# Kernel tuning notes

Hardware: AMD Instinct MI355X
Metric: run time of the kernel (lower is better)

The kernel has to match this reference:

```python
import jax, jax.numpy as jnp
import numpy as np

V, D, H, B, S = 50257, 256, 512, 64, 512


def setup_inputs() -> dict:
    key = jax.random.key(0)
    ks = jax.random.split(key, 6)
    rn = lambda k, shp, sc: (jax.random.normal(k, shp, jnp.float32) * sc)
    return {
        "tokens": jax.random.randint(ks[0], (B, S), 0, V, dtype=jnp.int32),
        "emb": rn(ks[1], (V, D), 0.05),        # embedding table
        "W": rn(ks[2], (D, 3 * H), 0.05),       # input kernel, gate order [z,r,h]
        "U": rn(ks[3], (H, 3 * H), 0.05),       # recurrent kernel
        "b": jnp.zeros((2, 3 * H), jnp.float32),  # (input_bias, recurrent_bias), reset_after=True
        "Wd": rn(ks[4], (H, V), 0.02),          # dense kernel
        "bd": jnp.zeros((V,), jnp.float32),
    }


def _gru_last_state(tokens, emb, W, U, b):
    # mask_zero=True: steps where token==0 carry state forward unchanged
    mask = tokens != 0                         # [B,S]
    x = emb[tokens]                            # [B,S,D] embedding gather
    xp = x @ W + b[0]                          # [B,S,3H] precomputed input projections
    xz, xr, xh = jnp.split(xp, 3, axis=-1)

    def step(h, inp):
        xz_t, xr_t, xh_t, m_t = inp            # [B,H]x3, [B]
        rec = h @ U + b[1]                     # recurrent projection with recurrent bias
        rz, rr, rh = jnp.split(rec, 3, axis=-1)
        z = jax.nn.sigmoid(xz_t + rz)          # update gate
        r = jax.nn.sigmoid(xr_t + rr)          # reset gate
        hh = jnp.tanh(xh_t + r * rh)           # candidate (reset_after=True)
        h_new = z * h + (1.0 - z) * hh
        h = jnp.where(m_t[:, None], h_new, h)  # masked steps keep previous state
        return h, None

    h0 = jnp.zeros((tokens.shape[0], U.shape[0]), xp.dtype)
    # scan over time: [S,B,H] layout
    h_last, _ = jax.lax.scan(
        step, h0,
        (xz.transpose(1, 0, 2), xr.transpose(1, 0, 2), xh.transpose(1, 0, 2), mask.T),
    )
    return h_last                              # [B,H]


def reference(tokens, emb, W, U, b, Wd, bd):
    h_last = _gru_last_state(tokens, emb, W, U, b)
    return jax.nn.softmax(h_last @ Wd + bd, axis=-1)  # [B,V]
```

## Files before the change

kernel.cpp:

```cpp
#include <hip/hip_runtime.h>
#include <hip/hip_bf16.h>

#define VV 50257
#define DD 256
#define HH 512
#define BB 64
#define SS 512
#define H3 1536
#define NWG 32
#define NSL 16
#define SCOLS 32
#define UCOLS 96
#define UBYTES (64*UCOLS*16)
#define SCRB 2048
#define HBYTES (BB*HH*2)

typedef _Float16 f16x8 __attribute__((ext_vector_type(8)));
typedef _Float16 f16x4 __attribute__((ext_vector_type(4)));
typedef float f32x4 __attribute__((ext_vector_type(4)));
typedef unsigned int u32x4 __attribute__((ext_vector_type(4)));
typedef unsigned int u32x2 __attribute__((ext_vector_type(2)));

#define AS1 __attribute__((address_space(1)))
#define AS3 __attribute__((address_space(3)))
#define GLL16(g, s) __builtin_amdgcn_global_load_lds((const AS1 char*)(g), (AS3 char*)(s), 16, 0, 0)

__global__ __launch_bounds__(256) void kPackW(const float* __restrict__ W,
                                              _Float16* __restrict__ wsW) {
    int idx = blockIdx.x * 256 + threadIdx.x;
    int kb = idx / H3, col = idx % H3;
    f16x8 v;
    #pragma unroll
    for (int e = 0; e < 8; ++e) v[e] = (_Float16)W[(size_t)(kb*8+e)*H3 + col];
    *(f16x8*)(wsW + (size_t)idx*8) = v;
}

__global__ __launch_bounds__(256) void kPackU(const float* __restrict__ U,
                                              _Float16* __restrict__ wsU) {
    int s = blockIdx.x;
    for (int idx = threadIdx.x; idx < 64*UCOLS; idx += 256) {
        int kb = idx / UCOLS, pc = idx % UCOLS;
        int gi = pc / SCOLS, cl = pc % SCOLS;
        int gcol = gi*HH + s*SCOLS + cl;
        f16x8 v;
        #pragma unroll
        for (int e = 0; e < 8; ++e) v[e] = (_Float16)U[(size_t)(kb*8+e)*H3 + gcol];
        *(f16x8*)(wsU + (size_t)s*(UBYTES/2) + (size_t)idx*8) = v;
    }
}

__global__ __launch_bounds__(256) void kMask(const int* __restrict__ tokens,
                                             unsigned long long* __restrict__ mb) {
    int t = blockIdx.x * 256 + threadIdx.x;
    if (t < SS) {
        unsigned long long m = 0ull;
        for (int r = 0; r < BB; ++r)
            m |= (unsigned long long)(tokens[r*SS + t] != 0) << r;
        mb[t] = m;
    }
}

__global__ __launch_bounds__(256) void k1_embed_proj(
    const int* __restrict__ tokens, const float* __restrict__ emb,
    const _Float16* __restrict__ wsW, const float* __restrict__ bias,
    _Float16* __restrict__ xp)
{
    const int s  = blockIdx.y;
    const int nt = blockIdx.x;
    const int tid = threadIdx.x;
    __shared__ _Float16 aLds[64 * 256];

    for (int c = tid; c < 64 * 32; c += 256) {
        int row = c >> 5, kc = c & 31;
        int tok = tokens[row * SS + s];
        const float* src = emb + (size_t)tok * DD + kc * 8;
        float4 f0 = *(const float4*)(src);
        float4 f1 = *(const float4*)(src + 4);
        f16x8 v;
        v[0]=(_Float16)f0.x; v[1]=(_Float16)f0.y; v[2]=(_Float16)f0.z; v[3]=(_Float16)f0.w;
        v[4]=(_Float16)f1.x; v[5]=(_Float16)f1.y; v[6]=(_Float16)f1.z; v[7]=(_Float16)f1.w;
        int byte = row * 512 + ((kc * 16) ^ ((row & 7) << 4));
        *(f16x8*)((char*)aLds + byte) = v;
    }
    __syncthreads();

    const int w = tid >> 6, l = tid & 63;
    const int l15 = l & 15, lk = l >> 4;
    const int colbase = nt * 128;
    f32x4 acc[8] = {};

    for (int ks = 0; ks < 8; ++ks) {
        int arow = 16 * w + l15;
        f16x8 aF = *(const f16x8*)((const char*)aLds + arow*512 + (((ks*32 + lk*8)*2) ^ ((arow & 7) << 4)));
        int kb = ks*4 + lk;
        #pragma unroll
        for (int ns = 0; ns < 8; ++ns) {
            int col = colbase + ns * 16 + l15;
            f16x8 bF = *(const f16x8*)(wsW + ((size_t)kb * H3 + col) * 8);
            acc[ns] = __builtin_amdgcn_mfma_f32_16x16x32_f16(aF, bF, acc[ns], 0, 0, 0);
        }
    }
    #pragma unroll
    for (int ns = 0; ns < 8; ++ns) {
        int col = colbase + ns * 16 + l15;
        float b0 = bias[col];
        f16x4 vv;
        #pragma unroll
        for (int i = 0; i < 4; ++i) vv[i] = (_Float16)(acc[ns][i] + b0);
        *(f16x4*)(xp + ((size_t)s * H3 + col) * BB + 16*w + lk*4) = vv;
    }
}

__global__ __launch_bounds__(256) void k2_scan(
    const _Float16* __restrict__ xp, const _Float16* __restrict__ wsU,
    const float* __restrict__ bias, const unsigned long long* __restrict__ maskbits,
    char* __restrict__ hpub, float* __restrict__ hlast,
    unsigned int* __restrict__ flags)
{
    extern __shared__ char uLds[];
    const int tid = threadIdx.x;
    const int g = blockIdx.x >> 4;
    const int s = blockIdx.x & 15;
    const int w = tid >> 6, l = tid & 63;
    const int l15 = l & 15, lk = l >> 4;
    const int mi = w >> 1, c = w & 1;
    const int rb = g*32 + mi*16;
    const int j  = s*SCOLS + c*16 + l15;
    const int b0 = rb + lk*4;
    const int cluster = (g*2 + mi) << 5;
    unsigned short* scr = (unsigned short*)(uLds + UBYTES + w*512);

    {
        const char* src = (const char*)wsU + (size_t)s * UBYTES;
        #pragma unroll
        for (int base = 0; base < UBYTES; base += 4096)
            GLL16(src + base + tid*16, uLds + base + tid*16);
    }

    f16x4 xpe0, xpe1, xpe2, xpo0, xpo1, xpo2;
    unsigned long long mbe, mbo;
    {
        const _Float16* x0 = xp;
        xpe0 = *(const f16x4*)(x0 + (0*HH + j)*BB + b0);
        xpe1 = *(const f16x4*)(x0 + (1*HH + j)*BB + b0);
        xpe2 = *(const f16x4*)(x0 + (2*HH + j)*BB + b0);
        const _Float16* x1 = xp + (size_t)H3 * BB;
        xpo0 = *(const f16x4*)(x1 + (0*HH + j)*BB + b0);
        xpo1 = *(const f16x4*)(x1 + (1*HH + j)*BB + b0);
        xpo2 = *(const f16x4*)(x1 + (2*HH + j)*BB + b0);
        mbe = maskbits[0];
        mbo = maskbits[1];
    }
    const float b1z = bias[H3 + j];
    const float b1r = bias[H3 + HH + j];
    const float b1h = bias[H3 + 2*HH + j];
    float hold[4] = {};
    __syncthreads();

    auto step = [&](int t, f16x4 xz4, f16x4 xr4, f16x4 xh4,
                    unsigned long long mbv) __attribute__((always_inline)) {
        f32x4 az = {}, ar = {}, ah = {};
        if (t > 0) {
            {
                const unsigned int* fp = flags + (cluster + (l & 31)) * 16;
                int n = 0;
                bool ok;
                do {
                    unsigned v = __hip_atomic_load(fp, __ATOMIC_RELAXED,
                                                   __HIP_MEMORY_SCOPE_AGENT);
                    ok = __all((int)(v >= (unsigned)t));
                } while (!ok && ++n < 100000);
            }
            const unsigned expm = ((t >> 1) & 1) ? 0x40004000u : 0u;
            const char* hsrc = hpub + (size_t)(t & 1) * HBYTES;
            unsigned long long hb = (unsigned long long)(hsrc + (rb + l15)*1024 + lk*16);
            u32x4 hf[16];
            int n = 0;
            while (true) {
#define LDH(i, off) asm volatile("global_load_dwordx4 %0, %1, off offset:" off " sc0 sc1" \
                                 : "=v"(hf[i]) : "v"(hb) : "memory")
                LDH(0,"0");    LDH(1,"64");   LDH(2,"128");  LDH(3,"192");
                LDH(4,"256");  LDH(5,"320");  LDH(6,"384");  LDH(7,"448");
                LDH(8,"512");  LDH(9,"576");  LDH(10,"640"); LDH(11,"704");
                LDH(12,"768"); LDH(13,"832"); LDH(14,"896"); LDH(15,"960");
#undef LDH
                asm volatile("s_waitcnt vmcnt(0)" ::: "memory");
                __builtin_amdgcn_sched_barrier(0);
                unsigned st = 0;
                #pragma unroll
                for (int p = 0; p < 16; ++p) {
                    #pragma unroll
                    for (int d = 0; d < 4; ++d)
                        st |= (hf[p][d] & 0x40004000u) ^ expm;
                }
                if (!__any((int)(st != 0))) break;
                if (++n > 2000) break;
            }
            #pragma unroll
            for (int p = 0; p < 16; ++p) {
                #pragma unroll
                for (int d = 0; d < 4; ++d) hf[p][d] &= 0xBFFFBFFFu;
            }
            __builtin_amdgcn_sched_barrier(0);
            #pragma unroll
            for (int ks = 0; ks < 16; ++ks) {
                f16x8 a = __builtin_bit_cast(f16x8, hf[ks]);
                const char* ub = uLds + (size_t)((ks*4 + lk)*UCOLS + c*16 + l15) * 16;
                f16x8 bz = *(const f16x8*)(ub);
                f16x8 br = *(const f16x8*)(ub + 512);
                f16x8 bh = *(const f16x8*)(ub + 1024);
                az = __builtin_amdgcn_mfma_f32_16x16x32_f16(a, bz, az, 0, 0, 0);
                ar = __builtin_amdgcn_mfma_f32_16x16x32_f16(a, br, ar, 0, 0, 0);
                ah = __builtin_amdgcn_mfma_f32_16x16x32_f16(a, bh, ah, 0, 0, 0);
            }
        }
        #pragma unroll
        for (int i = 0; i < 4; ++i) {
            int row = b0 + i;
            float z  = 1.f / (1.f + __expf(-((float)xz4[i] + az[i] + b1z)));
            float rg = 1.f / (1.f + __expf(-((float)xr4[i] + ar[i] + b1r)));
            float ag = (float)xh4[i] + rg * (ah[i] + b1h);
            float hc = 1.f - 2.f / (__expf(2.f * ag) + 1.f);
            float hn = z * hold[i] + (1.f - z) * hc;
            if (!((mbv >> row) & 1ull)) hn = hold[i];
            hold[i] = hn;
        }
        if (t < SS - 1) {
            const unsigned tg = (((unsigned)(t + 1) >> 1) & 1u) << 14;
            #pragma unroll
            for (int i = 0; i < 4; ++i) {
                unsigned hb16 = (unsigned)__builtin_bit_cast(unsigned short, (_Float16)hold[i]);
                if ((hb16 & 0x7FFFu) >= 0x3C00u) hb16 = (hb16 & 0x8000u) | 0x3BFFu;
                scr[(lk*4 + i)*16 + l15] = (unsigned short)(hb16 | tg);
            }
            u32x2 pk = *(const u32x2*)(scr + (l >> 2)*16 + (l & 3)*4);
            char* hnxt = hpub + (size_t)((t + 1) & 1) * HBYTES;
            unsigned long long pa = (unsigned long long)
                (hnxt + (size_t)(rb + (l >> 2))*1024 + (size_t)(s*SCOLS + c*16 + (l & 3)*4)*2);
            asm volatile("global_store_dwordx2 %0, %1, off sc0 sc1"
                         :: "v"(pa), "v"(pk) : "memory");
            if (l == 0)
                __hip_atomic_store(flags + (cluster + (s*2 + c)) * 16,
                                   (unsigned)(t + 1),
                                   __ATOMIC_RELAXED, __HIP_MEMORY_SCOPE_AGENT);
        } else {
            #pragma unroll
            for (int i = 0; i < 4; ++i)
                hlast[(b0 + i)*HH + j] = hold[i];
        }
    };

    for (int t = 0; t < SS; t += 2) {
        step(t, xpe0, xpe1, xpe2, mbe);
        {
            int tl = (t + 2 < SS) ? t + 2 : SS - 1;
            const _Float16* xt = xp + (size_t)tl * H3 * BB;
            xpe0 = *(const f16x4*)(xt + (0*HH + j)*BB + b0);
            xpe1 = *(const f16x4*)(xt + (1*HH + j)*BB + b0);
            xpe2 = *(const f16x4*)(xt + (2*HH + j)*BB + b0);
            mbe = maskbits[tl];
        }
        step(t + 1, xpo0, xpo1, xpo2, mbo);
        {
            int tl = (t + 3 < SS) ? t + 3 : SS - 1;
            const _Float16* xt = xp + (size_t)tl * H3 * BB;
            xpo0 = *(const f16x4*)(xt + (0*HH + j)*BB + b0);
            xpo1 = *(const f16x4*)(xt + (1*HH + j)*BB + b0);
            xpo2 = *(const f16x4*)(xt + (2*HH + j)*BB + b0);
            mbo = maskbits[tl];
        }
    }
}

__global__ __launch_bounds__(256) void k3_logits(
    const float* __restrict__ hin, const float* __restrict__ Wd,
    const float* __restrict__ bd, float* __restrict__ out,
    float* __restrict__ partials)
{
    const int nt = blockIdx.x;
    const int tid = threadIdx.x;
    __shared__ _Float16 hLds[64 * 512];

    for (int c = tid; c < 64 * 64; c += 256) {
        int row = c >> 6, kc = c & 63;
        const float* src = hin + row * HH + kc * 8;
        float4 f0 = *(const float4*)(src);
        float4 f1 = *(const float4*)(src + 4);
        f16x8 v;
        v[0]=(_Float16)f0.x; v[1]=(_Float16)f0.y; v[2]=(_Float16)f0.z; v[3]=(_Float16)f0.w;
        v[4]=(_Float16)f1.x; v[5]=(_Float16)f1.y; v[6]=(_Float16)f1.z; v[7]=(_Float16)f1.w;
        int byte = row * 1024 + ((kc * 16) ^ ((row & 7) << 4));
        *(f16x8*)((char*)hLds + byte) = v;
    }
    __syncthreads();

    const int w = tid >> 6, l = tid & 63;
    const int l15 = l & 15, lk = l >> 4;
    f32x4 acc[8] = {};

    for (int ks = 0; ks < 16; ++ks) {
        int arow = 16 * w + l15;
        int abyte = arow * 1024 + ((((ks * 32 + lk * 8) * 2)) ^ ((arow & 7) << 4));
        f16x8 aFrag = *(const f16x8*)((const char*)hLds + abyte);
        int krow = ks * 32 + lk * 8;
        #pragma unroll
        for (int ns = 0; ns < 8; ++ns) {
            int col = nt * 128 + ns * 16 + l15;
            f16x8 bFrag;
            if (col < VV) {
                #pragma unroll
                for (int i = 0; i < 8; ++i) bFrag[i] = (_Float16)Wd[(size_t)(krow + i) * VV + col];
            } else {
                #pragma unroll
                for (int i = 0; i < 8; ++i) bFrag[i] = (_Float16)0.f;
            }
            acc[ns] = __builtin_amdgcn_mfma_f32_16x16x32_f16(aFrag, bFrag, acc[ns], 0, 0, 0);
        }
    }

    float lg[8][4];
    float m[4] = {-3.4e38f, -3.4e38f, -3.4e38f, -3.4e38f};
    float ss[4] = {0.f, 0.f, 0.f, 0.f};
    #pragma unroll
    for (int ns = 0; ns < 8; ++ns) {
        int col = nt * 128 + ns * 16 + l15;
        bool ok = col < VV;
        float bv = ok ? bd[col] : 0.f;
        #pragma unroll
        for (int i = 0; i < 4; ++i) {
            int row = 16 * w + lk * 4 + i;
            float v = acc[ns][i] + bv;
            lg[ns][i] = ok ? v : -3.4e38f;
            if (ok) {
                out[(size_t)row * VV + col] = v;
                m[i] = fmaxf(m[i], v);
            }
        }
    }
    #pragma unroll
    for (int i = 0; i < 4; ++i) {
        #pragma unroll
        for (int ns = 0; ns < 8; ++ns)
            if (lg[ns][i] > -3.3e38f) ss[i] += __expf(lg[ns][i] - m[i]);
        for (int d = 1; d < 16; d <<= 1) {
            float m2 = __shfl_xor(m[i], d);
            float s2 = __shfl_xor(ss[i], d);
            float nM = fmaxf(m[i], m2);
            ss[i] = ss[i] * __expf(m[i] - nM) + s2 * __expf(m2 - nM);
            m[i] = nM;
        }
        if (l15 == 0) {
            int row = 16 * w + lk * 4 + i;
            partials[((size_t)nt * 64 + row) * 2 + 0] = m[i];
            partials[((size_t)nt * 64 + row) * 2 + 1] = ss[i];
        }
    }
}

__global__ __launch_bounds__(64) void k3_reduce(
    const float* __restrict__ partials, float* __restrict__ rowMS)
{
    int row = blockIdx.x, l = threadIdx.x;
    float M = -3.4e38f, Ssum = 0.f;
    for (int p = l; p < 393; p += 64) {
        float mp = partials[((size_t)p * 64 + row) * 2 + 0];
        float sp = partials[((size_t)p * 64 + row) * 2 + 1];
        float nM = fmaxf(M, mp);
        Ssum = Ssum * __expf(M - nM) + sp * __expf(mp - nM);
        M = nM;
    }
    for (int d = 1; d < 64; d <<= 1) {
        float m2 = __shfl_xor(M, d), s2 = __shfl_xor(Ssum, d);
        float nM = fmaxf(M, m2);
        Ssum = Ssum * __expf(M - nM) + s2 * __expf(m2 - nM);
        M = nM;
    }
    if (l == 0) { rowMS[row * 2] = M; rowMS[row * 2 + 1] = Ssum; }
}

__global__ __launch_bounds__(256) void k3_softmax(
    float* __restrict__ out, const float* __restrict__ rowMS)
{
    int col = blockIdx.x * 256 + threadIdx.x;
    int row = blockIdx.y;
    if (col < VV) {
        float M = rowMS[row * 2], Sv = rowMS[row * 2 + 1];
        size_t idx = (size_t)row * VV + col;
        out[idx] = __expf(out[idx] - M) / Sv;
    }
}

extern "C" void kernel_launch(void* const* d_in, const int* in_sizes, int n_in,
                              void* d_out, int out_size, void* d_ws, size_t ws_size,
                              hipStream_t stream) {
    const int*   tokens = (const int*)  d_in[0];
    const float* emb    = (const float*)d_in[1];
    const float* W      = (const float*)d_in[2];
    const float* U      = (const float*)d_in[3];
    const float* bias   = (const float*)d_in[4];
    const float* Wd     = (const float*)d_in[5];
    const float* bd     = (const float*)d_in[6];
    float* out = (float*)d_out;

    const size_t XP_BYTES   = (size_t)SS * BB * H3 * 2;
    const size_t WSU_BYTES  = (size_t)NSL * UBYTES;
    const size_t WSW_BYTES  = (size_t)32 * H3 * 8 * 2;
    const size_t HPUB_BYTES = 2 * (size_t)HBYTES;
    const size_t HLAST_BYTES= (size_t)BB * HH * 4;
    const size_t MASK_BYTES = (size_t)SS * 8;
    const size_t FLAG_BYTES = 8192;
    const size_t PART_BYTES = (size_t)393 * 64 * 2 * 4;

    char* ws = (char*)d_ws;
    _Float16* xp    = (_Float16*)ws;
    _Float16* wsU   = (_Float16*)(ws + XP_BYTES);
    _Float16* wsW   = (_Float16*)(ws + XP_BYTES + WSU_BYTES);
    char*     hpub  =            ws + XP_BYTES + WSU_BYTES + WSW_BYTES;
    float*    hlast = (float*)  (hpub + HPUB_BYTES);
    unsigned long long* maskb = (unsigned long long*)(hpub + HPUB_BYTES + HLAST_BYTES);
    unsigned int* flags = (unsigned int*)(hpub + HPUB_BYTES + HLAST_BYTES + MASK_BYTES);
    float* partials = (float*)(hpub + HPUB_BYTES + HLAST_BYTES + MASK_BYTES + FLAG_BYTES);
    float* rowMS    = (float*)(hpub + HPUB_BYTES + HLAST_BYTES + MASK_BYTES + FLAG_BYTES + PART_BYTES);

    hipFuncSetAttribute((const void*)k2_scan,
                        hipFuncAttributeMaxDynamicSharedMemorySize, UBYTES + SCRB);

    hipMemsetAsync(hpub, 0x00, HBYTES, stream);
    hipMemsetAsync(hpub + HBYTES, 0x40, HBYTES, stream);
    hipMemsetAsync(flags, 0, FLAG_BYTES, stream);

    kPackW<<<32 * H3 / 256, 256, 0, stream>>>(W, wsW);
    kPackU<<<NSL, 256, 0, stream>>>(U, wsU);
    kMask<<<2, 256, 0, stream>>>(tokens, maskb);
    k1_embed_proj<<<dim3(12, 512), 256, 0, stream>>>(tokens, emb, wsW, bias, xp);

    k2_scan<<<NWG, 256, UBYTES + SCRB, stream>>>(xp, wsU, bias, maskb, hpub, hlast, flags);

    k3_logits<<<393, 256, 0, stream>>>(hlast, Wd, bd, out, partials);
    k3_reduce<<<64, 64, 0, stream>>>(partials, rowMS);
    k3_softmax<<<dim3((VV + 255) / 256, BB), 256, 0, stream>>>(out, rowMS);
}
```

Baseline: 2.511 ms.

## Consume recurrent state chunks as producer flags arrive instead of waiting for all

Replaces the wait-for-all-flags barrier plus full reload of the hidden state with an incremental loop. It polls per-producer flags, loads only the 16-byte chunks whose producer pair is ready, validates their parity tag, and issues the MFMAs for that chunk immediately. The aim is to overlap recurrent-matmul work with waiting on slower workgroups in the cross-workgroup step synchronization. In exchange it adds divergent control flow, many polling iterations with small loads, and possibly worse instruction scheduling than the straight-line unrolled MFMA chain.

Measured after the change: 3.110 ms. 1.24x slower.

```diff
diff --git a/kernel.cpp b/kernel.cpp
--- a/kernel.cpp
+++ b/kernel.cpp
@@ -161,58 +161,83 @@
                     unsigned long long mbv) __attribute__((always_inline)) {
         f32x4 az = {}, ar = {}, ah = {};
         if (t > 0) {
-            {
-                const unsigned int* fp = flags + (cluster + (l & 31)) * 16;
-                int n = 0;
-                bool ok;
-                do {
-                    unsigned v = __hip_atomic_load(fp, __ATOMIC_RELAXED,
-                                                   __HIP_MEMORY_SCOPE_AGENT);
-                    ok = __all((int)(v >= (unsigned)t));
-                } while (!ok && ++n < 100000);
-            }
             const unsigned expm = ((t >> 1) & 1) ? 0x40004000u : 0u;
             const char* hsrc = hpub + (size_t)(t & 1) * HBYTES;
             unsigned long long hb = (unsigned long long)(hsrc + (rb + l15)*1024 + lk*16);
             u32x4 hf[16];
+            const unsigned int* fp = flags + (cluster + (l & 31)) * 16;
+            unsigned done = 0;
             int n = 0;
-            while (true) {
+
 #define LDH(i, off) asm volatile("global_load_dwordx4 %0, %1, off offset:" off " sc0 sc1" \
                                  : "=v"(hf[i]) : "v"(hb) : "memory")
-                LDH(0,"0");    LDH(1,"64");   LDH(2,"128");  LDH(3,"192");
-                LDH(4,"256");  LDH(5,"320");  LDH(6,"384");  LDH(7,"448");
-                LDH(8,"512");  LDH(9,"576");  LDH(10,"640"); LDH(11,"704");
-                LDH(12,"768"); LDH(13,"832"); LDH(14,"896"); LDH(15,"960");
+#define VMF(p, uboff)                                                          \
+            if (newly & (1u << (p))) {                                         \
+                unsigned st = 0;                                               \
+                for (int d = 0; d < 4; ++d)                                    \
+                    st |= (hf[p][d] & 0x40004000u) ^ expm;                     \
+                if (!__any((int)(st != 0))) {                                  \
+                    for (int d = 0; d < 4; ++d) hf[p][d] &= 0xBFFFBFFFu;       \
+                    f16x8 a = __builtin_bit_cast(f16x8, hf[p]);                \
+                    const char* ub = uLds + (size_t)(uboff) + c*256 + l15*16;  \
+                    az = __builtin_amdgcn_mfma_f32_16x16x32_f16(a, *(const f16x8*)(ub), az, 0, 0, 0);          \
+                    ar = __builtin_amdgcn_mfma_f32_16x16x32_f16(a, *(const f16x8*)(ub + 512), ar, 0, 0, 0);    \
+                    ah = __builtin_amdgcn_mfma_f32_16x16x32_f16(a, *(const f16x8*)(ub + 1024), ah, 0, 0, 0);   \
+                    done |= 1u << (p);                                         \
+                }                                                              \
+            }
+
+            while (done != 0xFFFFu && n < 100000) {
+                unsigned v = __hip_atomic_load(fp, __ATOMIC_RELAXED,
+                                               __HIP_MEMORY_SCOPE_AGENT);
+                unsigned long long bal = __ballot((int)(v >= (unsigned)t));
+                unsigned b32 = (unsigned)bal;
+                unsigned pairs = b32 & (b32 >> 1) & 0x55555555u;
+                unsigned rm = 0;
+                #pragma unroll
+                for (int p = 0; p < 16; ++p) rm |= ((pairs >> (2*p)) & 1u) << p;
+                unsigned newly = (rm & ~done) | (done ^ done);
+                newly = rm & ~done;
+                if (newly) {
+                    if (newly & 1u<<0)  LDH(0,"0");
+                    if (newly & 1u<<1)  LDH(1,"64");
+                    if (newly & 1u<<2)  LDH(2,"128");
+                    if (newly & 1u<<3)  LDH(3,"192");
+                    if (newly & 1u<<4)  LDH(4,"256");
+                    if (newly & 1u<<5)  LDH(5,"320");
+                    if (newly & 1u<<6)  LDH(6,"384");
+                    if (newly & 1u<<7)  LDH(7,"448");
+                    if (newly & 1u<<8)  LDH(8,"512");
+                    if (newly & 1u<<9)  LDH(9,"576");
+                    if (newly & 1u<<10) LDH(10,"640");
+                    if (newly & 1u<<11) LDH(11,"704");
+                    if (newly & 1u<<12) LDH(12,"768");
+                    if (newly & 1u<<13) LDH(13,"832");
+                    if (newly & 1u<<14) LDH(14,"896");
+                    if (newly & 1u<<15) LDH(15,"960");
+                    asm volatile("s_waitcnt vmcnt(0)" ::: "memory");
+                    __builtin_amdgcn_sched_barrier(0);
+                    VMF(0,  (0*4 + lk)*UCOLS*16)
+                    VMF(1,  (1*4 + lk)*UCOLS*16)
+                    VMF(2,  (2*4 + lk)*UCOLS*16)
+                    VMF(3,  (3*4 + lk)*UCOLS*16)
+                    VMF(4,  (4*4 + lk)*UCOLS*16)
+                    VMF(5,  (5*4 + lk)*UCOLS*16)
+                    VMF(6,  (6*4 + lk)*UCOLS*16)
+                    VMF(7,  (7*4 + lk)*UCOLS*16)
+                    VMF(8,  (8*4 + lk)*UCOLS*16)
+                    VMF(9,  (9*4 + lk)*UCOLS*16)
+                    VMF(10, (10*4 + lk)*UCOLS*16)
+                    VMF(11, (11*4 + lk)*UCOLS*16)
+                    VMF(12, (12*4 + lk)*UCOLS*16)
+                    VMF(13, (13*4 + lk)*UCOLS*16)
+                    VMF(14, (14*4 + lk)*UCOLS*16)
+                    VMF(15, (15*4 + lk)*UCOLS*16)
+                }
+                ++n;
+            }
+#undef VMF
 #undef LDH
-                asm volatile("s_waitcnt vmcnt(0)" ::: "memory");
-                __builtin_amdgcn_sched_barrier(0);
-                unsigned st = 0;
-                #pragma unroll
-                for (int p = 0; p < 16; ++p) {
-                    #pragma unroll
-                    for (int d = 0; d < 4; ++d)
-                        st |= (hf[p][d] & 0x40004000u) ^ expm;
-                }
-                if (!__any((int)(st != 0))) break;
-                if (++n > 2000) break;
-            }
-            #pragma unroll
-            for (int p = 0; p < 16; ++p) {
-                #pragma unroll
-                for (int d = 0; d < 4; ++d) hf[p][d] &= 0xBFFFBFFFu;
-            }
-            __builtin_amdgcn_sched_barrier(0);
-            #pragma unroll
-            for (int ks = 0; ks < 16; ++ks) {
-                f16x8 a = __builtin_bit_cast(f16x8, hf[ks]);
-                const char* ub = uLds + (size_t)((ks*4 + lk)*UCOLS + c*16 + l15) * 16;
-                f16x8 bz = *(const f16x8*)(ub);
-                f16x8 br = *(const f16x8*)(ub + 512);
-                f16x8 bh = *(const f16x8*)(ub + 1024);
-                az = __builtin_amdgcn_mfma_f32_16x16x32_f16(a, bz, az, 0, 0, 0);
-                ar = __builtin_amdgcn_mfma_f32_16x16x32_f16(a, br, ar, 0, 0, 0);
-                ah = __builtin_amdgcn_mfma_f32_16x16x32_f16(a, bh, ah, 0, 0, 0);
-            }
         }
         #pragma unroll
         for (int i = 0; i < 4; ++i) {
```
